# Performance work log

Hardware: AMD Instinct MI355X
Metric: run time of the kernel (lower is better)

Reference implementation:

```python
import jax, jax.numpy as jnp
import numpy as np

HIDDEN = 2048
INTER = 5632
B, S = 2, 2048


def _ternary(key, shape):
    # values in {-1, 0, +1}, matching 2-bit packed ternary weights
    return jax.random.randint(key, shape, -1, 2).astype(jnp.float32)


def setup_inputs() -> dict:
    key = jax.random.key(0)
    ks = jax.random.split(key, 7)
    x = jax.random.normal(ks[0], (B, S, HIDDEN), dtype=jnp.float32)
    gate_w = _ternary(ks[1], (INTER, HIDDEN))   # [intermediate, hidden]
    up_w = _ternary(ks[2], (INTER, HIDDEN))     # [intermediate, hidden]
    down_w = _ternary(ks[3], (HIDDEN, INTER))   # [hidden, intermediate]
    # per-output-channel dequant scales (positive, as from absmean quantization)
    gate_s = jax.random.uniform(ks[4], (INTER,), minval=0.01, maxval=0.1, dtype=jnp.float32)
    up_s = jax.random.uniform(ks[5], (INTER,), minval=0.01, maxval=0.1, dtype=jnp.float32)
    down_s = jax.random.uniform(ks[6], (HIDDEN,), minval=0.01, maxval=0.1, dtype=jnp.float32)
    return {"x": x, "gate_w": gate_w, "up_w": up_w, "down_w": down_w,
            "gate_s": gate_s, "up_s": up_s, "down_s": down_s}


def reference(x, gate_w, up_w, down_w, gate_s, up_s, down_s):
    # x: (B, S, H) -> flatten tokens, as in forward_hidden
    b, s, h = x.shape
    xf = x.reshape(b * s, h)
    # ternary linear = add/sub-only matmul + per-channel scale
    g = jnp.einsum('th,ih->ti', xf, gate_w) * gate_s   # (T, I)
    u = jnp.einsum('th,ih->ti', xf, up_w) * up_s       # (T, I)
    hdn = jax.nn.silu(g) * u                            # gated activation
    out = jnp.einsum('ti,hi->th', hdn, down_w) * down_s  # (T, H)
    return out.reshape(b, s, -1)
```

## Files before the change

kernel.cpp:

```cpp
#include <hip/hip_runtime.h>
#include <stdint.h>
#include <stddef.h>

#define HIDDEN 2048
#define INTER  5632
#define TOKENS 4096
#define BK     64
#define BKI    128

typedef __attribute__((ext_vector_type(8))) _Float16 f16x8;
typedef __attribute__((ext_vector_type(4))) _Float16 f16x4;
typedef __attribute__((ext_vector_type(4))) float    f32x4;
typedef __attribute__((ext_vector_type(4))) int      i32x4;

__device__ __forceinline__ int swz8(int row, int q) {
    return row * 8 + ((q + row) & 7);
}

__global__ __launch_bounds__(256)
void prepass(const float* __restrict__ x,
             const float4* __restrict__ gw, const float4* __restrict__ uw,
             const float4* __restrict__ dw,
             int8_t* __restrict__ xq, float* __restrict__ xs,
             int* __restrict__ go, int* __restrict__ uo,
             f16x4* __restrict__ dno) {
    const int tid = threadIdx.x;
    if (blockIdx.x < TOKENS) {
        const int t = blockIdx.x;
        const float4* row = (const float4*)(x + (size_t)t * HIDDEN);
        float4 v0 = row[tid * 2];
        float4 v1 = row[tid * 2 + 1];
        float m = fmaxf(fmaxf(fabsf(v0.x), fabsf(v0.y)), fmaxf(fabsf(v0.z), fabsf(v0.w)));
        m = fmaxf(m, fmaxf(fmaxf(fabsf(v1.x), fabsf(v1.y)), fmaxf(fabsf(v1.z), fabsf(v1.w))));
        #pragma unroll
        for (int off = 32; off; off >>= 1)
            m = fmaxf(m, __shfl_xor(m, off, 64));
        __shared__ float wmax[4];
        if ((tid & 63) == 0) wmax[tid >> 6] = m;
        __syncthreads();
        m = fmaxf(fmaxf(wmax[0], wmax[1]), fmaxf(wmax[2], wmax[3]));
        m = fmaxf(m, 1e-20f);
        if (tid == 0) xs[t] = m * (1.0f / 127.0f);
        const float inv = 127.0f / m;
        float vals[8] = {v0.x, v0.y, v0.z, v0.w, v1.x, v1.y, v1.z, v1.w};
        int b[8];
        #pragma unroll
        for (int i = 0; i < 8; ++i) b[i] = (int)rintf(vals[i] * inv);
        int lo = (b[0] & 255) | ((b[1] & 255) << 8) | ((b[2] & 255) << 16) | (b[3] << 24);
        int hi = (b[4] & 255) | ((b[5] & 255) << 8) | ((b[6] & 255) << 16) | (b[7] << 24);
        ((int2*)(xq + (size_t)t * HIDDEN))[tid] = make_int2(lo, hi);
        return;
    }
    const int NW4 = INTER * HIDDEN / 4;
    int i = (blockIdx.x - TOKENS) * blockDim.x + tid;
    const int stride = 2048 * blockDim.x;
    for (; i < 3 * NW4; i += stride) {
        if (i < 2 * NW4) {
            const bool is_g = i < NW4;
            const int j = is_g ? i : i - NW4;
            float4 f = is_g ? gw[j] : uw[j];
            int p = ((int)(signed char)(int)f.x & 255)
                  | (((int)(signed char)(int)f.y & 255) << 8)
                  | (((int)(signed char)(int)f.z & 255) << 16)
                  | (((int)(signed char)(int)f.w) << 24);
            if (is_g) go[j] = p; else uo[j] = p;
        } else {
            const int j = i - 2 * NW4;
            float4 f = dw[j];
            f16x4 o;
            o.x = (_Float16)f.x; o.y = (_Float16)f.y;
            o.z = (_Float16)f.z; o.w = (_Float16)f.w;
            dno[j] = o;
        }
    }
}

__global__ __launch_bounds__(256, 2)
void gemm_gateup(const int8_t* __restrict__ Xq,
                 const int8_t* __restrict__ Wg,
                 const int8_t* __restrict__ Wu,
                 const float* __restrict__ xs,
                 const float* __restrict__ gs,
                 const float* __restrict__ us,
                 _Float16* __restrict__ Hm) {
    __shared__ int8_t As [128 * BKI];
    __shared__ int8_t Bgs[128 * BKI];
    __shared__ int8_t Bus[128 * BKI];

    const int pid   = blockIdx.x;
    const int local = pid % (16 * 44);
    const int bm    = ((pid / (16 * 44)) * 16 + (local & 15)) * 128;
    const int bn    = (local >> 4) * 128;

    const int tid  = threadIdx.x;
    const int lane = tid & 63;
    const int wave = tid >> 6;
    const int wm   = (wave >> 1) * 64;
    const int wn   = (wave & 1) * 64;
    const int l15  = lane & 15;
    const int lq   = lane >> 4;

    int rowA[4], sgA[4];
    #pragma unroll
    for (int j = 0; j < 4; ++j) {
        const int f = tid + 256 * j;
        rowA[j] = f >> 3;
        sgA[j]  = (((f & 7) - rowA[j]) & 7) * 16;
    }

    i32x4 accg[4][4] = {};
    i32x4 accu[4][4] = {};

    for (int k0 = 0; k0 < HIDDEN; k0 += BKI) {
        #pragma unroll
        for (int j = 0; j < 4; ++j) {
            const int f = tid + 256 * j;
            const int8_t* pX = Xq + (size_t)(bm + rowA[j]) * HIDDEN + k0 + sgA[j];
            const int8_t* pG = Wg + (size_t)(bn + rowA[j]) * HIDDEN + k0 + sgA[j];
            const int8_t* pU = Wu + (size_t)(bn + rowA[j]) * HIDDEN + k0 + sgA[j];
            __builtin_amdgcn_global_load_lds(
                (__attribute__((address_space(1))) void*)pX,
                (__attribute__((address_space(3))) void*)&As[f * 16], 16, 0, 0);
            __builtin_amdgcn_global_load_lds(
                (__attribute__((address_space(1))) void*)pG,
                (__attribute__((address_space(3))) void*)&Bgs[f * 16], 16, 0, 0);
            __builtin_amdgcn_global_load_lds(
                (__attribute__((address_space(1))) void*)pU,
                (__attribute__((address_space(3))) void*)&Bus[f * 16], 16, 0, 0);
        }
        __syncthreads();

        #pragma unroll
        for (int ks = 0; ks < 2; ++ks) {
            const int q = ks * 4 + lq;
            i32x4 a[4];
            #pragma unroll
            for (int im = 0; im < 4; ++im)
                a[im] = *(const i32x4*)&As[swz8(wm + im * 16 + l15, q) * 16];
            #pragma unroll
            for (int jn = 0; jn < 4; ++jn) {
                i32x4 bg = *(const i32x4*)&Bgs[swz8(wn + jn * 16 + l15, q) * 16];
                i32x4 bu = *(const i32x4*)&Bus[swz8(wn + jn * 16 + l15, q) * 16];
                #pragma unroll
                for (int im = 0; im < 4; ++im) {
                    accg[im][jn] = __builtin_amdgcn_mfma_i32_16x16x64_i8(a[im], bg, accg[im][jn], 0, 0, 0);
                    accu[im][jn] = __builtin_amdgcn_mfma_i32_16x16x64_i8(a[im], bu, accu[im][jn], 0, 0, 0);
                }
            }
        }
        __syncthreads();
    }

    #pragma unroll
    for (int jn = 0; jn < 4; ++jn) {
        const int col = bn + wn + jn * 16 + l15;
        const float sg = gs[col];
        const float su = us[col];
        #pragma unroll
        for (int im = 0; im < 4; ++im) {
            const int rbase = bm + wm + im * 16 + lq * 4;
            #pragma unroll
            for (int r = 0; r < 4; ++r) {
                const int row = rbase + r;
                const float st = xs[row];
                float g = (float)accg[im][jn][r] * st * sg;
                float u = (float)accu[im][jn][r] * st * su;
                float h = (g / (1.0f + __expf(-g))) * u;
                Hm[(size_t)row * INTER + col] = (_Float16)h;
            }
        }
    }
}

__global__ __launch_bounds__(256, 2)
void gemm_down(const _Float16* __restrict__ Hm,
               const _Float16* __restrict__ Wd,
               const float* __restrict__ dsc,
               float* __restrict__ out) {
    __shared__ _Float16 As[128 * BK];
    __shared__ _Float16 Bs[128 * BK];

    const int pid = blockIdx.x;
    const int loc = pid & 255;
    const int bm  = ((pid >> 8) * 16 + (loc & 15)) * 128;
    const int bn  = (loc >> 4) * 128;

    const int tid  = threadIdx.x;
    const int lane = tid & 63;
    const int wave = tid >> 6;
    const int wm   = (wave >> 1) * 64;
    const int wn   = (wave & 1) * 64;
    const int l15  = lane & 15;
    const int lq   = lane >> 4;

    int rowA[4], sgA[4];
    #pragma unroll
    for (int j = 0; j < 4; ++j) {
        const int f = tid + 256 * j;
        rowA[j] = f >> 3;
        sgA[j]  = (((f & 7) - rowA[j]) & 7) * 8;
    }

    f32x4 acc[4][4] = {};

    for (int k0 = 0; k0 < INTER; k0 += BK) {
        #pragma unroll
        for (int j = 0; j < 4; ++j) {
            const int f = tid + 256 * j;
            const _Float16* pA = Hm + (size_t)(bm + rowA[j]) * INTER + k0 + sgA[j];
            const _Float16* pB = Wd + (size_t)(bn + rowA[j]) * INTER + k0 + sgA[j];
            __builtin_amdgcn_global_load_lds(
                (__attribute__((address_space(1))) void*)pA,
                (__attribute__((address_space(3))) void*)&As[f * 8], 16, 0, 0);
            __builtin_amdgcn_global_load_lds(
                (__attribute__((address_space(1))) void*)pB,
                (__attribute__((address_space(3))) void*)&Bs[f * 8], 16, 0, 0);
        }
        __syncthreads();

        #pragma unroll
        for (int ks = 0; ks < 2; ++ks) {
            const int q = ks * 4 + lq;
            f16x8 a[4];
            #pragma unroll
            for (int im = 0; im < 4; ++im)
                a[im] = *(const f16x8*)&As[swz8(wm + im * 16 + l15, q) * 8];
            #pragma unroll
            for (int jn = 0; jn < 4; ++jn) {
                f16x8 b = *(const f16x8*)&Bs[swz8(wn + jn * 16 + l15, q) * 8];
                #pragma unroll
                for (int im = 0; im < 4; ++im)
                    acc[im][jn] = __builtin_amdgcn_mfma_f32_16x16x32_f16(a[im], b, acc[im][jn], 0, 0, 0);
            }
        }
        __syncthreads();
    }

    #pragma unroll
    for (int jn = 0; jn < 4; ++jn) {
        const int col = bn + wn + jn * 16 + l15;
        const float sd = dsc[col];
        #pragma unroll
        for (int im = 0; im < 4; ++im) {
            const int rbase = bm + wm + im * 16 + lq * 4;
            #pragma unroll
            for (int r = 0; r < 4; ++r)
                out[(size_t)(rbase + r) * HIDDEN + col] = acc[im][jn][r] * sd;
        }
    }
}

extern "C" void kernel_launch(void* const* d_in, const int* in_sizes, int n_in,
                              void* d_out, int out_size, void* d_ws, size_t ws_size,
                              hipStream_t stream) {
    const float* x   = (const float*)d_in[0];
    const float* gw  = (const float*)d_in[1];
    const float* uw  = (const float*)d_in[2];
    const float* dw  = (const float*)d_in[3];
    const float* gsc = (const float*)d_in[4];
    const float* usc = (const float*)d_in[5];
    const float* dsc = (const float*)d_in[6];
    float* out = (float*)d_out;

    char* ws = (char*)d_ws;
    int8_t*   Xq  = (int8_t*)(ws);
    int8_t*   Wg8 = (int8_t*)(ws + 8388608ull);
    int8_t*   Wu8 = (int8_t*)(ws + 19922944ull);
    _Float16* Wdh = (_Float16*)(ws + 31457280ull);
    _Float16* Hm  = (_Float16*)(ws + 54525952ull);
    float*    xs  = (float*)(ws + 100663296ull);

    prepass<<<TOKENS + 2048, 256, 0, stream>>>(
        x, (const float4*)gw, (const float4*)uw, (const float4*)dw,
        Xq, xs, (int*)Wg8, (int*)Wu8, (f16x4*)Wdh);

    gemm_gateup<<<(INTER / 128) * (TOKENS / 128), 256, 0, stream>>>(
        Xq, Wg8, Wu8, xs, gsc, usc, Hm);
    gemm_down<<<(HIDDEN / 128) * (TOKENS / 128), 256, 0, stream>>>(
        Hm, Wdh, dsc, out);
}
```

Baseline: 376.5 us.

## Add triple-buffered LDS pipeline to both GEMMs and enlarge down-proj tiles

Both GEMM kernels now use a three-stage LDS ring buffer with async global-to-LDS loads issued two tiles ahead. Staging is split into halves interleaved with MFMA phases, using explicit vmcnt/lgkmcnt waits, raw barriers and setprio in place of full __syncthreads. The gate/up kernel drops its K-tile from 128 to 64 bytes to fit three buffers. The down kernel moves to 512 threads with 256x128 tiles and a remapped block order, meant to raise B-tile reuse and hide memory latency. The trade-offs are more LDS per block, which may lower occupancy, and fragile hand-counted wait values.

```diff
diff --git a/kernel.cpp b/kernel.cpp
--- a/kernel.cpp
+++ b/kernel.cpp
@@ -6,16 +6,21 @@
 #define INTER  5632
 #define TOKENS 4096
 #define BK     64
-#define BKI    128
+#define NT_GU  (HIDDEN / BK)
+#define NT_DN  (INTER / BK)
 
 typedef __attribute__((ext_vector_type(8))) _Float16 f16x8;
 typedef __attribute__((ext_vector_type(4))) _Float16 f16x4;
 typedef __attribute__((ext_vector_type(4))) float    f32x4;
 typedef __attribute__((ext_vector_type(4))) int      i32x4;
 
-__device__ __forceinline__ int swz8(int row, int q) {
-    return row * 8 + ((q + row) & 7);
-}
+__device__ __forceinline__ int swz8(int row, int q) { return row * 8 + ((q + row) & 7); }
+__device__ __forceinline__ int swz4(int row, int q) { return row * 4 + ((q + row) & 3); }
+__device__ __forceinline__ int rot3(int i) { return i == 2 ? 0 : i + 1; }
+
+#define GLDS16(g, l) __builtin_amdgcn_global_load_lds( \
+    (__attribute__((address_space(1))) void*)(g), \
+    (__attribute__((address_space(3))) void*)(l), 16, 0, 0)
 
 __global__ __launch_bounds__(256)
 void prepass(const float* __restrict__ x,
@@ -83,9 +88,9 @@
                  const float* __restrict__ gs,
                  const float* __restrict__ us,
                  _Float16* __restrict__ Hm) {
-    __shared__ int8_t As [128 * BKI];
-    __shared__ int8_t Bgs[128 * BKI];
-    __shared__ int8_t Bus[128 * BKI];
+    __shared__ int8_t As [3][128 * BK];
+    __shared__ int8_t Bgs[3][128 * BK];
+    __shared__ int8_t Bus[3][128 * BK];
 
     const int pid   = blockIdx.x;
     const int local = pid % (16 * 44);
@@ -100,56 +105,90 @@
     const int l15  = lane & 15;
     const int lq   = lane >> 4;
 
-    int rowA[4], sgA[4];
+    int rowS[2], segS[2];
     #pragma unroll
-    for (int j = 0; j < 4; ++j) {
+    for (int j = 0; j < 2; ++j) {
         const int f = tid + 256 * j;
-        rowA[j] = f >> 3;
-        sgA[j]  = (((f & 7) - rowA[j]) & 7) * 16;
-    }
+        rowS[j] = f >> 2;
+        segS[j] = (((f & 3) - (f >> 2)) & 3) * 16;
+    }
+
+    const int8_t* gA = Xq + (size_t)bm * HIDDEN;
+    const int8_t* gG = Wg + (size_t)bn * HIDDEN;
+    const int8_t* gU = Wu + (size_t)bn * HIDDEN;
 
     i32x4 accg[4][4] = {};
     i32x4 accu[4][4] = {};
 
-    for (int k0 = 0; k0 < HIDDEN; k0 += BKI) {
-        #pragma unroll
-        for (int j = 0; j < 4; ++j) {
-            const int f = tid + 256 * j;
-            const int8_t* pX = Xq + (size_t)(bm + rowA[j]) * HIDDEN + k0 + sgA[j];
-            const int8_t* pG = Wg + (size_t)(bn + rowA[j]) * HIDDEN + k0 + sgA[j];
-            const int8_t* pU = Wu + (size_t)(bn + rowA[j]) * HIDDEN + k0 + sgA[j];
-            __builtin_amdgcn_global_load_lds(
-                (__attribute__((address_space(1))) void*)pX,
-                (__attribute__((address_space(3))) void*)&As[f * 16], 16, 0, 0);
-            __builtin_amdgcn_global_load_lds(
-                (__attribute__((address_space(1))) void*)pG,
-                (__attribute__((address_space(3))) void*)&Bgs[f * 16], 16, 0, 0);
-            __builtin_amdgcn_global_load_lds(
-                (__attribute__((address_space(1))) void*)pU,
-                (__attribute__((address_space(3))) void*)&Bus[f * 16], 16, 0, 0);
-        }
-        __syncthreads();
-
-        #pragma unroll
-        for (int ks = 0; ks < 2; ++ks) {
-            const int q = ks * 4 + lq;
-            i32x4 a[4];
-            #pragma unroll
-            for (int im = 0; im < 4; ++im)
-                a[im] = *(const i32x4*)&As[swz8(wm + im * 16 + l15, q) * 16];
-            #pragma unroll
-            for (int jn = 0; jn < 4; ++jn) {
-                i32x4 bg = *(const i32x4*)&Bgs[swz8(wn + jn * 16 + l15, q) * 16];
-                i32x4 bu = *(const i32x4*)&Bus[swz8(wn + jn * 16 + l15, q) * 16];
-                #pragma unroll
-                for (int im = 0; im < 4; ++im) {
-                    accg[im][jn] = __builtin_amdgcn_mfma_i32_16x16x64_i8(a[im], bg, accg[im][jn], 0, 0, 0);
-                    accu[im][jn] = __builtin_amdgcn_mfma_i32_16x16x64_i8(a[im], bu, accu[im][jn], 0, 0, 0);
-                }
+    #define STG_GU(b, t, j) do { \
+        const int f_ = tid + 256 * (j); \
+        const size_t off_ = (size_t)rowS[j] * HIDDEN + (size_t)(t) * BK + segS[j]; \
+        GLDS16(gA + off_, &As [b][f_ * 16]); \
+        GLDS16(gG + off_, &Bgs[b][f_ * 16]); \
+        GLDS16(gU + off_, &Bus[b][f_ * 16]); \
+    } while (0)
+
+    STG_GU(0, 0, 0); STG_GU(0, 0, 1);
+    STG_GU(1, 1, 0); STG_GU(1, 1, 1);
+    asm volatile("s_waitcnt vmcnt(6)" ::: "memory");
+    __builtin_amdgcn_s_barrier();
+    __builtin_amdgcn_sched_barrier(0);
+
+    int cur = 0, stg = 2;
+    for (int t = 0; t < NT_GU; ++t) {
+        const int8_t* A_ = As [cur];
+        const int8_t* G_ = Bgs[cur];
+        const int8_t* U_ = Bus[cur];
+
+        if (t + 2 < NT_GU) STG_GU(stg, t + 2, 0);
+        i32x4 a[4], b0[2], b1[2];
+        #pragma unroll
+        for (int im = 0; im < 4; ++im)
+            a[im] = *(const i32x4*)&A_[swz4(wm + im * 16 + l15, lq) * 16];
+        #pragma unroll
+        for (int jn = 0; jn < 2; ++jn) {
+            b0[jn] = *(const i32x4*)&G_[swz4(wn + jn * 16 + l15, lq) * 16];
+            b1[jn] = *(const i32x4*)&U_[swz4(wn + jn * 16 + l15, lq) * 16];
+        }
+        __builtin_amdgcn_s_barrier();
+        asm volatile("s_waitcnt lgkmcnt(0)");
+        __builtin_amdgcn_s_setprio(1);
+        #pragma unroll
+        for (int jn = 0; jn < 2; ++jn)
+            #pragma unroll
+            for (int im = 0; im < 4; ++im) {
+                accg[im][jn] = __builtin_amdgcn_mfma_i32_16x16x64_i8(a[im], b0[jn], accg[im][jn], 0, 0, 0);
+                accu[im][jn] = __builtin_amdgcn_mfma_i32_16x16x64_i8(a[im], b1[jn], accu[im][jn], 0, 0, 0);
             }
-        }
-        __syncthreads();
-    }
+        __builtin_amdgcn_s_setprio(0);
+        __builtin_amdgcn_s_barrier();
+
+        if (t + 2 < NT_GU) STG_GU(stg, t + 2, 1);
+        #pragma unroll
+        for (int jn = 0; jn < 2; ++jn) {
+            b0[jn] = *(const i32x4*)&G_[swz4(wn + (jn + 2) * 16 + l15, lq) * 16];
+            b1[jn] = *(const i32x4*)&U_[swz4(wn + (jn + 2) * 16 + l15, lq) * 16];
+        }
+        __builtin_amdgcn_s_barrier();
+        asm volatile("s_waitcnt lgkmcnt(0)");
+        __builtin_amdgcn_s_setprio(1);
+        #pragma unroll
+        for (int jn = 0; jn < 2; ++jn)
+            #pragma unroll
+            for (int im = 0; im < 4; ++im) {
+                accg[im][jn + 2] = __builtin_amdgcn_mfma_i32_16x16x64_i8(a[im], b0[jn], accg[im][jn + 2], 0, 0, 0);
+                accu[im][jn + 2] = __builtin_amdgcn_mfma_i32_16x16x64_i8(a[im], b1[jn], accu[im][jn + 2], 0, 0, 0);
+            }
+        __builtin_amdgcn_s_setprio(0);
+
+        if (t < NT_GU - 2)       { asm volatile("s_waitcnt vmcnt(6)" ::: "memory"); }
+        else if (t == NT_GU - 2) { asm volatile("s_waitcnt vmcnt(0)" ::: "memory"); }
+        __builtin_amdgcn_s_barrier();
+        __builtin_amdgcn_sched_barrier(0);
+
+        cur = rot3(cur); stg = rot3(stg);
+    }
+    #undef STG_GU
 
     #pragma unroll
     for (int jn = 0; jn < 4; ++jn) {
@@ -172,18 +211,18 @@
     }
 }
 
-__global__ __launch_bounds__(256, 2)
+__global__ __launch_bounds__(512, 2)
 void gemm_down(const _Float16* __restrict__ Hm,
                const _Float16* __restrict__ Wd,
                const float* __restrict__ dsc,
                float* __restrict__ out) {
-    __shared__ _Float16 As[128 * BK];
-    __shared__ _Float16 Bs[128 * BK];
+    __shared__ _Float16 As[3][256 * BK];
+    __shared__ _Float16 Bs[3][128 * BK];
 
     const int pid = blockIdx.x;
-    const int loc = pid & 255;
-    const int bm  = ((pid >> 8) * 16 + (loc & 15)) * 128;
-    const int bn  = (loc >> 4) * 128;
+    const int p2  = (pid & 7) * 32 + (pid >> 3);
+    const int bm  = (p2 & 15) * 256;
+    const int bn  = (p2 >> 4) * 128;
 
     const int tid  = threadIdx.x;
     const int lane = tid & 63;
@@ -193,48 +232,91 @@
     const int l15  = lane & 15;
     const int lq   = lane >> 4;
 
-    int rowA[4], sgA[4];
+    int rS[4], sS[4];
     #pragma unroll
     for (int j = 0; j < 4; ++j) {
-        const int f = tid + 256 * j;
-        rowA[j] = f >> 3;
-        sgA[j]  = (((f & 7) - rowA[j]) & 7) * 8;
-    }
+        const int f = tid + 512 * j;
+        rS[j] = f >> 3;
+        sS[j] = (((f & 7) - (f >> 3)) & 7) * 8;
+    }
+
+    const _Float16* gA = Hm + (size_t)bm * INTER;
+    const _Float16* gB = Wd + (size_t)bn * INTER;
 
     f32x4 acc[4][4] = {};
 
-    for (int k0 = 0; k0 < INTER; k0 += BK) {
-        #pragma unroll
-        for (int j = 0; j < 4; ++j) {
-            const int f = tid + 256 * j;
-            const _Float16* pA = Hm + (size_t)(bm + rowA[j]) * INTER + k0 + sgA[j];
-            const _Float16* pB = Wd + (size_t)(bn + rowA[j]) * INTER + k0 + sgA[j];
-            __builtin_amdgcn_global_load_lds(
-                (__attribute__((address_space(1))) void*)pA,
-                (__attribute__((address_space(3))) void*)&As[f * 8], 16, 0, 0);
-            __builtin_amdgcn_global_load_lds(
-                (__attribute__((address_space(1))) void*)pB,
-                (__attribute__((address_space(3))) void*)&Bs[f * 8], 16, 0, 0);
-        }
-        __syncthreads();
-
-        #pragma unroll
-        for (int ks = 0; ks < 2; ++ks) {
-            const int q = ks * 4 + lq;
-            f16x8 a[4];
+    #define STG_DA(b, t, j) do { \
+        const int f_ = tid + 512 * (j); \
+        GLDS16(gA + (size_t)rS[j] * INTER + (size_t)(t) * BK + sS[j], &As[b][f_ * 8]); \
+    } while (0)
+    #define STG_DB(b, t, j) do { \
+        const int f_ = tid + 512 * (j); \
+        GLDS16(gB + (size_t)rS[j] * INTER + (size_t)(t) * BK + sS[j], &Bs[b][f_ * 8]); \
+    } while (0)
+
+    STG_DA(0, 0, 0); STG_DA(0, 0, 1); STG_DA(0, 0, 2); STG_DA(0, 0, 3);
+    STG_DB(0, 0, 0); STG_DB(0, 0, 1);
+    STG_DA(1, 1, 0); STG_DA(1, 1, 1); STG_DA(1, 1, 2); STG_DA(1, 1, 3);
+    STG_DB(1, 1, 0); STG_DB(1, 1, 1);
+    asm volatile("s_waitcnt vmcnt(6)" ::: "memory");
+    __builtin_amdgcn_s_barrier();
+    __builtin_amdgcn_sched_barrier(0);
+
+    int cur = 0, stg = 2;
+    for (int t = 0; t < NT_DN; ++t) {
+        const _Float16* A_ = As[cur];
+        const _Float16* B_ = Bs[cur];
+
+        if (t + 2 < NT_DN) { STG_DA(stg, t + 2, 0); STG_DA(stg, t + 2, 1); STG_DB(stg, t + 2, 0); }
+        {
+            f16x8 a[4], b[4];
             #pragma unroll
             for (int im = 0; im < 4; ++im)
-                a[im] = *(const f16x8*)&As[swz8(wm + im * 16 + l15, q) * 8];
-            #pragma unroll
-            for (int jn = 0; jn < 4; ++jn) {
-                f16x8 b = *(const f16x8*)&Bs[swz8(wn + jn * 16 + l15, q) * 8];
+                a[im] = *(const f16x8*)&A_[swz8(wm + im * 16 + l15, lq) * 8];
+            #pragma unroll
+            for (int jn = 0; jn < 4; ++jn)
+                b[jn] = *(const f16x8*)&B_[swz8(wn + jn * 16 + l15, lq) * 8];
+            __builtin_amdgcn_s_barrier();
+            asm volatile("s_waitcnt lgkmcnt(0)");
+            __builtin_amdgcn_s_setprio(1);
+            #pragma unroll
+            for (int jn = 0; jn < 4; ++jn)
                 #pragma unroll
                 for (int im = 0; im < 4; ++im)
-                    acc[im][jn] = __builtin_amdgcn_mfma_f32_16x16x32_f16(a[im], b, acc[im][jn], 0, 0, 0);
-            }
-        }
-        __syncthreads();
-    }
+                    acc[im][jn] = __builtin_amdgcn_mfma_f32_16x16x32_f16(a[im], b[jn], acc[im][jn], 0, 0, 0);
+            __builtin_amdgcn_s_setprio(0);
+            __builtin_amdgcn_s_barrier();
+        }
+
+        if (t + 2 < NT_DN) { STG_DA(stg, t + 2, 2); STG_DA(stg, t + 2, 3); STG_DB(stg, t + 2, 1); }
+        {
+            f16x8 a[4], b[4];
+            #pragma unroll
+            for (int im = 0; im < 4; ++im)
+                a[im] = *(const f16x8*)&A_[swz8(wm + im * 16 + l15, 4 + lq) * 8];
+            #pragma unroll
+            for (int jn = 0; jn < 4; ++jn)
+                b[jn] = *(const f16x8*)&B_[swz8(wn + jn * 16 + l15, 4 + lq) * 8];
+            __builtin_amdgcn_s_barrier();
+            asm volatile("s_waitcnt lgkmcnt(0)");
+            __builtin_amdgcn_s_setprio(1);
+            #pragma unroll
+            for (int jn = 0; jn < 4; ++jn)
+                #pragma unroll
+                for (int im = 0; im < 4; ++im)
+                    acc[im][jn] = __builtin_amdgcn_mfma_f32_16x16x32_f16(a[im], b[jn], acc[im][jn], 0, 0, 0);
+            __builtin_amdgcn_s_setprio(0);
+        }
+
+        if (t < NT_DN - 2)       { asm volatile("s_waitcnt vmcnt(6)" ::: "memory"); }
+        else if (t == NT_DN - 2) { asm volatile("s_waitcnt vmcnt(0)" ::: "memory"); }
+        __builtin_amdgcn_s_barrier();
+        __builtin_amdgcn_sched_barrier(0);
+
+        cur = rot3(cur); stg = rot3(stg);
+    }
+    #undef STG_DA
+    #undef STG_DB
 
     #pragma unroll
     for (int jn = 0; jn < 4; ++jn) {
@@ -276,6 +358,6 @@
 
     gemm_gateup<<<(INTER / 128) * (TOKENS / 128), 256, 0, stream>>>(
         Xq, Wg8, Wu8, xs, gsc, usc, Hm);
-    gemm_down<<<(HIDDEN / 128) * (TOKENS / 128), 256, 0, stream>>>(
+    gemm_down<<<(HIDDEN / 128) * (TOKENS / 256), 512, 0, stream>>>(
         Hm, Wdh, dsc, out);
 }
```

Measured after the change: 477.9 us. +26.9%, slower.

## Shrink gate/up K-tile and split down GEMM into 128x64 tiles for occupancy

Applied to the files above, without the earlier changes.

The gate/up int8 GEMM drops its K tile from 128 to 64 bytes and uses a new LDS swizzle that pairs rows, which halves shared memory per block so four blocks can share a CU. The down GEMM moves to 128-thread blocks covering 128x64 output tiles, doubling the block count with the launch bound changed to allow three blocks per CU. The aim is more resident waves to hide memory latency. In exchange there are twice as many K iterations and barriers in gate/up, and the narrower down tiles reload the A operand more often.

```diff
diff --git a/kernel.cpp b/kernel.cpp
--- a/kernel.cpp
+++ b/kernel.cpp
@@ -6,16 +6,21 @@
 #define INTER  5632
 #define TOKENS 4096
 #define BK     64
-#define BKI    128
 
 typedef __attribute__((ext_vector_type(8))) _Float16 f16x8;
 typedef __attribute__((ext_vector_type(4))) _Float16 f16x4;
 typedef __attribute__((ext_vector_type(4))) float    f32x4;
 typedef __attribute__((ext_vector_type(4))) int      i32x4;
 
-__device__ __forceinline__ int swz8(int row, int q) {
-    return row * 8 + ((q + row) & 7);
-}
+__device__ __forceinline__ int swz8(int row, int q) { return row * 8 + ((q + row) & 7); }
+
+__device__ __forceinline__ int slotGU(int m, int q) {
+    return (m >> 1) * 8 + (m & 1) * 4 + ((q + (m >> 1)) & 3);
+}
+
+#define GLDS16(g, l) __builtin_amdgcn_global_load_lds( \
+    (__attribute__((address_space(1))) void*)(g), \
+    (__attribute__((address_space(3))) void*)(l), 16, 0, 0)
 
 __global__ __launch_bounds__(256)
 void prepass(const float* __restrict__ x,
@@ -75,7 +80,7 @@
     }
 }
 
-__global__ __launch_bounds__(256, 2)
+__global__ __launch_bounds__(256, 4)
 void gemm_gateup(const int8_t* __restrict__ Xq,
                  const int8_t* __restrict__ Wg,
                  const int8_t* __restrict__ Wu,
@@ -83,9 +88,9 @@
                  const float* __restrict__ gs,
                  const float* __restrict__ us,
                  _Float16* __restrict__ Hm) {
-    __shared__ int8_t As [128 * BKI];
-    __shared__ int8_t Bgs[128 * BKI];
-    __shared__ int8_t Bus[128 * BKI];
+    __shared__ int8_t As [128 * BK];
+    __shared__ int8_t Bgs[128 * BK];
+    __shared__ int8_t Bus[128 * BK];
 
     const int pid   = blockIdx.x;
     const int local = pid % (16 * 44);
@@ -100,52 +105,40 @@
     const int l15  = lane & 15;
     const int lq   = lane >> 4;
 
-    int rowA[4], sgA[4];
-    #pragma unroll
-    for (int j = 0; j < 4; ++j) {
+    int rowS[2], segS[2];
+    #pragma unroll
+    for (int j = 0; j < 2; ++j) {
         const int f = tid + 256 * j;
-        rowA[j] = f >> 3;
-        sgA[j]  = (((f & 7) - rowA[j]) & 7) * 16;
+        rowS[j] = 2 * (f >> 3) + ((f >> 2) & 1);
+        segS[j] = (((f & 3) - (f >> 3)) & 3) * 16;
     }
 
     i32x4 accg[4][4] = {};
     i32x4 accu[4][4] = {};
 
-    for (int k0 = 0; k0 < HIDDEN; k0 += BKI) {
-        #pragma unroll
-        for (int j = 0; j < 4; ++j) {
+    for (int k0 = 0; k0 < HIDDEN; k0 += BK) {
+        #pragma unroll
+        for (int j = 0; j < 2; ++j) {
             const int f = tid + 256 * j;
-            const int8_t* pX = Xq + (size_t)(bm + rowA[j]) * HIDDEN + k0 + sgA[j];
-            const int8_t* pG = Wg + (size_t)(bn + rowA[j]) * HIDDEN + k0 + sgA[j];
-            const int8_t* pU = Wu + (size_t)(bn + rowA[j]) * HIDDEN + k0 + sgA[j];
-            __builtin_amdgcn_global_load_lds(
-                (__attribute__((address_space(1))) void*)pX,
-                (__attribute__((address_space(3))) void*)&As[f * 16], 16, 0, 0);
-            __builtin_amdgcn_global_load_lds(
-                (__attribute__((address_space(1))) void*)pG,
-                (__attribute__((address_space(3))) void*)&Bgs[f * 16], 16, 0, 0);
-            __builtin_amdgcn_global_load_lds(
-                (__attribute__((address_space(1))) void*)pU,
-                (__attribute__((address_space(3))) void*)&Bus[f * 16], 16, 0, 0);
-        }
-        __syncthreads();
-
-        #pragma unroll
-        for (int ks = 0; ks < 2; ++ks) {
-            const int q = ks * 4 + lq;
-            i32x4 a[4];
-            #pragma unroll
-            for (int im = 0; im < 4; ++im)
-                a[im] = *(const i32x4*)&As[swz8(wm + im * 16 + l15, q) * 16];
-            #pragma unroll
-            for (int jn = 0; jn < 4; ++jn) {
-                i32x4 bg = *(const i32x4*)&Bgs[swz8(wn + jn * 16 + l15, q) * 16];
-                i32x4 bu = *(const i32x4*)&Bus[swz8(wn + jn * 16 + l15, q) * 16];
-                #pragma unroll
-                for (int im = 0; im < 4; ++im) {
-                    accg[im][jn] = __builtin_amdgcn_mfma_i32_16x16x64_i8(a[im], bg, accg[im][jn], 0, 0, 0);
-                    accu[im][jn] = __builtin_amdgcn_mfma_i32_16x16x64_i8(a[im], bu, accu[im][jn], 0, 0, 0);
-                }
+            const size_t off = (size_t)rowS[j] * HIDDEN + k0 + segS[j];
+            GLDS16(Xq + (size_t)bm * HIDDEN + off, &As [f * 16]);
+            GLDS16(Wg + (size_t)bn * HIDDEN + off, &Bgs[f * 16]);
+            GLDS16(Wu + (size_t)bn * HIDDEN + off, &Bus[f * 16]);
+        }
+        __syncthreads();
+
+        i32x4 a[4];
+        #pragma unroll
+        for (int im = 0; im < 4; ++im)
+            a[im] = *(const i32x4*)&As[slotGU(wm + im * 16 + l15, lq) * 16];
+        #pragma unroll
+        for (int jn = 0; jn < 4; ++jn) {
+            i32x4 bg = *(const i32x4*)&Bgs[slotGU(wn + jn * 16 + l15, lq) * 16];
+            i32x4 bu = *(const i32x4*)&Bus[slotGU(wn + jn * 16 + l15, lq) * 16];
+            #pragma unroll
+            for (int im = 0; im < 4; ++im) {
+                accg[im][jn] = __builtin_amdgcn_mfma_i32_16x16x64_i8(a[im], bg, accg[im][jn], 0, 0, 0);
+                accu[im][jn] = __builtin_amdgcn_mfma_i32_16x16x64_i8(a[im], bu, accu[im][jn], 0, 0, 0);
             }
         }
         __syncthreads();
@@ -172,49 +165,46 @@
     }
 }
 
-__global__ __launch_bounds__(256, 2)
+__global__ __launch_bounds__(128, 3)
 void gemm_down(const _Float16* __restrict__ Hm,
                const _Float16* __restrict__ Wd,
                const float* __restrict__ dsc,
                float* __restrict__ out) {
     __shared__ _Float16 As[128 * BK];
-    __shared__ _Float16 Bs[128 * BK];
+    __shared__ _Float16 Bs[ 64 * BK];
 
     const int pid = blockIdx.x;
-    const int loc = pid & 255;
-    const int bm  = ((pid >> 8) * 16 + (loc & 15)) * 128;
-    const int bn  = (loc >> 4) * 128;
+    const int loc = pid & 511;
+    const int bm  = ((pid >> 9) * 16 + (loc & 15)) * 128;
+    const int bn  = (loc >> 4) * 64;
 
     const int tid  = threadIdx.x;
     const int lane = tid & 63;
     const int wave = tid >> 6;
-    const int wm   = (wave >> 1) * 64;
-    const int wn   = (wave & 1) * 64;
+    const int wm   = wave * 64;
     const int l15  = lane & 15;
     const int lq   = lane >> 4;
 
-    int rowA[4], sgA[4];
-    #pragma unroll
-    for (int j = 0; j < 4; ++j) {
-        const int f = tid + 256 * j;
-        rowA[j] = f >> 3;
-        sgA[j]  = (((f & 7) - rowA[j]) & 7) * 8;
+    int rS[8], sS[8];
+    #pragma unroll
+    for (int j = 0; j < 8; ++j) {
+        const int f = tid + 128 * j;
+        rS[j] = f >> 3;
+        sS[j] = (((f & 7) - (f >> 3)) & 7) * 8;
     }
 
     f32x4 acc[4][4] = {};
 
     for (int k0 = 0; k0 < INTER; k0 += BK) {
         #pragma unroll
+        for (int j = 0; j < 8; ++j) {
+            const int f = tid + 128 * j;
+            GLDS16(Hm + (size_t)(bm + rS[j]) * INTER + k0 + sS[j], &As[f * 8]);
+        }
+        #pragma unroll
         for (int j = 0; j < 4; ++j) {
-            const int f = tid + 256 * j;
-            const _Float16* pA = Hm + (size_t)(bm + rowA[j]) * INTER + k0 + sgA[j];
-            const _Float16* pB = Wd + (size_t)(bn + rowA[j]) * INTER + k0 + sgA[j];
-            __builtin_amdgcn_global_load_lds(
-                (__attribute__((address_space(1))) void*)pA,
-                (__attribute__((address_space(3))) void*)&As[f * 8], 16, 0, 0);
-            __builtin_amdgcn_global_load_lds(
-                (__attribute__((address_space(1))) void*)pB,
-                (__attribute__((address_space(3))) void*)&Bs[f * 8], 16, 0, 0);
+            const int f = tid + 128 * j;
+            GLDS16(Wd + (size_t)(bn + rS[j]) * INTER + k0 + sS[j], &Bs[f * 8]);
         }
         __syncthreads();
 
@@ -227,7 +217,7 @@
                 a[im] = *(const f16x8*)&As[swz8(wm + im * 16 + l15, q) * 8];
             #pragma unroll
             for (int jn = 0; jn < 4; ++jn) {
-                f16x8 b = *(const f16x8*)&Bs[swz8(wn + jn * 16 + l15, q) * 8];
+                f16x8 b = *(const f16x8*)&Bs[swz8(jn * 16 + l15, q) * 8];
                 #pragma unroll
                 for (int im = 0; im < 4; ++im)
                     acc[im][jn] = __builtin_amdgcn_mfma_f32_16x16x32_f16(a[im], b, acc[im][jn], 0, 0, 0);
@@ -238,7 +228,7 @@
 
     #pragma unroll
     for (int jn = 0; jn < 4; ++jn) {
-        const int col = bn + wn + jn * 16 + l15;
+        const int col = bn + jn * 16 + l15;
         const float sd = dsc[col];
         #pragma unroll
         for (int im = 0; im < 4; ++im) {
@@ -276,6 +266,6 @@
 
     gemm_gateup<<<(INTER / 128) * (TOKENS / 128), 256, 0, stream>>>(
         Xq, Wg8, Wu8, xs, gsc, usc, Hm);
-    gemm_down<<<(HIDDEN / 128) * (TOKENS / 128), 256, 0, stream>>>(
+    gemm_down<<<(HIDDEN / 128) * (TOKENS / 64), 128, 0, stream>>>(
         Hm, Wdh, dsc, out);
 }
```

After: 1.127 ms. 2.99x slower.
